# Performance work log

Measured on AMD Instinct MI355X. Metric: run time of the kernel, lower is better.

## Reference

```python
import jax, jax.numpy as jnp
import numpy as np

DIM = 128
N = 1024


def setup_inputs() -> dict:
    key = jax.random.key(0)
    ks = jax.random.split(key, 11)
    s = 1.0 / np.sqrt(DIM)
    # Linear params stored as [in, out] (y = x @ W + b), matching torch math.
    return {
        "x": jax.random.normal(ks[0], (N, DIM), jnp.float32),
        "W_Q": jax.random.uniform(ks[1], (DIM, DIM), jnp.float32, -s, s),
        "b_Q": jax.random.uniform(ks[2], (DIM,), jnp.float32, -s, s),
        "W_K": jax.random.uniform(ks[3], (DIM, DIM), jnp.float32, -s, s),
        "b_K": jax.random.uniform(ks[4], (DIM,), jnp.float32, -s, s),
        "W_V": jax.random.uniform(ks[5], (DIM, DIM), jnp.float32, -s, s),
        "b_V": jax.random.uniform(ks[6], (DIM,), jnp.float32, -s, s),
        "W_Ev": jax.random.uniform(ks[7], (DIM, DIM), jnp.float32, -s, s),
        "b_Ev": jax.random.uniform(ks[8], (DIM,), jnp.float32, -s, s),
        "W_A": jax.random.uniform(ks[9], (DIM, 1), jnp.float32, -s, s),
        "b_A": jax.random.uniform(ks[10], (1,), jnp.float32, -s, s),
    }


def reference(x, W_Q, b_Q, W_K, b_K, W_V, b_V, W_Ev, b_Ev, W_A, b_A):
    Q = x @ W_Q + b_Q                               # [n, d]
    K = x @ W_K + b_K                               # [n, d]
    V = x @ W_V + b_V                               # [n, d]
    edge_feat = jax.nn.relu(Q[:, None, :] + K[None, :, :])   # [n, n, d]
    e_ij = jnp.squeeze(edge_feat @ W_A, -1) + b_A[0]          # [n, n]
    alpha = jax.nn.softmax(e_ij, axis=1)                      # softmax over j
    EV = edge_feat @ W_Ev + b_Ev                              # [n, n, d]
    # out_i = sum_j alpha_ij * (V_j + EV_ij)
    out = jnp.einsum('ij,ijd->id', alpha, V[None, :, :] + EV)
    return out
```

## Files before the change

### kernel.cpp

```cpp
#include <hip/hip_runtime.h>

#define N 1024
#define DIM 128
#define TI 4
#define JCH 128
#define NCH 8
#define SC 16
#define NSC 8

template <int CTRL>
__device__ __forceinline__ float dpp_add(float x) {
  int y = __builtin_amdgcn_update_dpp(0, __float_as_int(x), CTRL, 0xF, 0xF, true);
  return x + __int_as_float(y);
}
__device__ __forceinline__ float red32(float x) {
  x = dpp_add<0x111>(x);
  x = dpp_add<0x112>(x);
  x = dpp_add<0x114>(x);
  x = dpp_add<0x118>(x);
  x = dpp_add<0x142>(x);
  return x;
}

__device__ __forceinline__ float bcast32(float x, bool hi) {
  const float a = __int_as_float(__builtin_amdgcn_readlane(__float_as_int(x), 31));
  const float b = __int_as_float(__builtin_amdgcn_readlane(__float_as_int(x), 63));
  return hi ? b : a;
}

__device__ __forceinline__ float epart(const float4 q, const float4 k,
                                       const float4 w) {
  float a = fmaxf(q.x + k.x, 0.f) * w.x;
  a = fmaf(fmaxf(q.y + k.y, 0.f), w.y, a);
  a = fmaf(fmaxf(q.z + k.z, 0.f), w.z, a);
  a = fmaf(fmaxf(q.w + k.w, 0.f), w.w, a);
  return a;
}

__global__ __launch_bounds__(256) void qkv_kernel2(
    const float* __restrict__ x,
    const float* __restrict__ WQ, const float* __restrict__ bQ,
    const float* __restrict__ WK, const float* __restrict__ bK,
    const float* __restrict__ WV, const float* __restrict__ bV,
    float* __restrict__ Q, float* __restrict__ K, float* __restrict__ V) {
  const int i0 = blockIdx.x * 2;
  const int t = threadIdx.x;
  const int dq = t & 31;
  const int g = t >> 5;
  const int r = g & 1;
  const int qr = g >> 1;

  __shared__ __align__(16) float xs[2][DIM];
  __shared__ __align__(16) float pacc[4][3][2][DIM];

  if (t < 64) {
    const int row = t >> 5, c4 = t & 31;
    ((float4*)&xs[row][0])[c4] = ((const float4*)(x + (i0 + row) * DIM))[c4];
  }
  __syncthreads();

  const float4* WQ4 = (const float4*)WQ;
  const float4* WK4 = (const float4*)WK;
  const float4* WV4 = (const float4*)WV;
  float4 aQ = make_float4(0.f, 0.f, 0.f, 0.f);
  float4 aK = make_float4(0.f, 0.f, 0.f, 0.f);
  float4 aV = make_float4(0.f, 0.f, 0.f, 0.f);
  const int cbase = 32 * qr;
  for (int cc = 0; cc < 32; ++cc) {
    const int c = cbase + cc;
    const float xv = xs[r][c];
    const float4 wq = WQ4[c * 32 + dq];
    const float4 wk = WK4[c * 32 + dq];
    const float4 wv = WV4[c * 32 + dq];
    aQ.x = fmaf(xv, wq.x, aQ.x); aQ.y = fmaf(xv, wq.y, aQ.y);
    aQ.z = fmaf(xv, wq.z, aQ.z); aQ.w = fmaf(xv, wq.w, aQ.w);
    aK.x = fmaf(xv, wk.x, aK.x); aK.y = fmaf(xv, wk.y, aK.y);
    aK.z = fmaf(xv, wk.z, aK.z); aK.w = fmaf(xv, wk.w, aK.w);
    aV.x = fmaf(xv, wv.x, aV.x); aV.y = fmaf(xv, wv.y, aV.y);
    aV.z = fmaf(xv, wv.z, aV.z); aV.w = fmaf(xv, wv.w, aV.w);
  }
  ((float4*)&pacc[qr][0][r][0])[dq] = aQ;
  ((float4*)&pacc[qr][1][r][0])[dq] = aK;
  ((float4*)&pacc[qr][2][r][0])[dq] = aV;
  __syncthreads();

  {
    const int row = t >> 7, d = t & 127;
    const float q = (pacc[0][0][row][d] + pacc[1][0][row][d]) +
                    (pacc[2][0][row][d] + pacc[3][0][row][d]) + bQ[d];
    const float k = (pacc[0][1][row][d] + pacc[1][1][row][d]) +
                    (pacc[2][1][row][d] + pacc[3][1][row][d]) + bK[d];
    const float v = (pacc[0][2][row][d] + pacc[1][2][row][d]) +
                    (pacc[2][2][row][d] + pacc[3][2][row][d]) + bV[d];
    Q[(i0 + row) * DIM + d] = q;
    K[(i0 + row) * DIM + d] = k;
    V[(i0 + row) * DIM + d] = v;
  }
}

__global__ __launch_bounds__(256) void attn_fused4(
    const float* __restrict__ Q, const float* __restrict__ K,
    const float* __restrict__ V, const float* __restrict__ WA,
    float* __restrict__ Rw, float* __restrict__ Sw, float* __restrict__ Lw) {
  const int bi = blockIdx.x >> 3;
  const int jc = blockIdx.x & 7;
  const int i0 = bi * TI;
  const int j0 = jc * JCH;
  const int t = threadIdx.x;
  const int dq = t & 31;
  const int f = t >> 5;
  const bool hi = (t & 32) != 0;

  __shared__ __align__(16) float red_s[8 * TI * DIM];
  __shared__ __align__(16) float4 lred4[8];

  const float4 wa4 = ((const float4*)WA)[dq];
  float4 q4[TI];
#pragma unroll
  for (int r = 0; r < TI; ++r)
    q4[r] = ((const float4*)(Q + (i0 + r) * DIM))[dq];

  float4 Racc[TI], Sacc[TI];
#pragma unroll
  for (int r = 0; r < TI; ++r) {
    Racc[r] = make_float4(0.f, 0.f, 0.f, 0.f);
    Sacc[r] = make_float4(0.f, 0.f, 0.f, 0.f);
  }
  float4 lacc = make_float4(0.f, 0.f, 0.f, 0.f);

  float4 kc0 = ((const float4*)(K + (j0 + f) * DIM))[dq];
  float4 kc1 = ((const float4*)(K + (j0 + 8 + f) * DIM))[dq];
  float4 vc0 = ((const float4*)(V + (j0 + f) * DIM))[dq];
  float4 vc1 = ((const float4*)(V + (j0 + 8 + f) * DIM))[dq];

  for (int sc = 0; sc < NSC; ++sc) {
    float4 pe0, pe1;
    pe0.x = epart(q4[0], kc0, wa4); pe0.y = epart(q4[1], kc0, wa4);
    pe0.z = epart(q4[2], kc0, wa4); pe0.w = epart(q4[3], kc0, wa4);
    pe1.x = epart(q4[0], kc1, wa4); pe1.y = epart(q4[1], kc1, wa4);
    pe1.z = epart(q4[2], kc1, wa4); pe1.w = epart(q4[3], kc1, wa4);

    const int scn = (sc + 1 < NSC) ? sc + 1 : sc;
    const int jb = j0 + scn * SC;
    const float4 kn0 = ((const float4*)(K + (jb + f) * DIM))[dq];
    const float4 kn1 = ((const float4*)(K + (jb + 8 + f) * DIM))[dq];
    const float4 vn0 = ((const float4*)(V + (jb + f) * DIM))[dq];
    const float4 vn1 = ((const float4*)(V + (jb + 8 + f) * DIM))[dq];

    pe0.x = red32(pe0.x); pe0.y = red32(pe0.y);
    pe0.z = red32(pe0.z); pe0.w = red32(pe0.w);
    pe1.x = red32(pe1.x); pe1.y = red32(pe1.y);
    pe1.z = red32(pe1.z); pe1.w = red32(pe1.w);

    float4 p0, p1;
    p0.x = __expf(bcast32(pe0.x, hi)); p0.y = __expf(bcast32(pe0.y, hi));
    p0.z = __expf(bcast32(pe0.z, hi)); p0.w = __expf(bcast32(pe0.w, hi));
    p1.x = __expf(bcast32(pe1.x, hi)); p1.y = __expf(bcast32(pe1.y, hi));
    p1.z = __expf(bcast32(pe1.z, hi)); p1.w = __expf(bcast32(pe1.w, hi));

    {
      const float pr0[4] = {p0.x, p0.y, p0.z, p0.w};
      const float pr1[4] = {p1.x, p1.y, p1.z, p1.w};
#pragma unroll
      for (int r = 0; r < TI; ++r) {
        const float pa = pr0[r], pb = pr1[r];
        Racc[r].x = fmaf(pa, fmaxf(q4[r].x + kc0.x, 0.f), Racc[r].x);
        Racc[r].y = fmaf(pa, fmaxf(q4[r].y + kc0.y, 0.f), Racc[r].y);
        Racc[r].z = fmaf(pa, fmaxf(q4[r].z + kc0.z, 0.f), Racc[r].z);
        Racc[r].w = fmaf(pa, fmaxf(q4[r].w + kc0.w, 0.f), Racc[r].w);
        Racc[r].x = fmaf(pb, fmaxf(q4[r].x + kc1.x, 0.f), Racc[r].x);
        Racc[r].y = fmaf(pb, fmaxf(q4[r].y + kc1.y, 0.f), Racc[r].y);
        Racc[r].z = fmaf(pb, fmaxf(q4[r].z + kc1.z, 0.f), Racc[r].z);
        Racc[r].w = fmaf(pb, fmaxf(q4[r].w + kc1.w, 0.f), Racc[r].w);
        Sacc[r].x = fmaf(pa, vc0.x, Sacc[r].x);
        Sacc[r].y = fmaf(pa, vc0.y, Sacc[r].y);
        Sacc[r].z = fmaf(pa, vc0.z, Sacc[r].z);
        Sacc[r].w = fmaf(pa, vc0.w, Sacc[r].w);
        Sacc[r].x = fmaf(pb, vc1.x, Sacc[r].x);
        Sacc[r].y = fmaf(pb, vc1.y, Sacc[r].y);
        Sacc[r].z = fmaf(pb, vc1.z, Sacc[r].z);
        Sacc[r].w = fmaf(pb, vc1.w, Sacc[r].w);
      }
      lacc.x += p0.x + p1.x; lacc.y += p0.y + p1.y;
      lacc.z += p0.z + p1.z; lacc.w += p0.w + p1.w;
    }

    kc0 = kn0; kc1 = kn1; vc0 = vn0; vc1 = vn1;
  }

  float4* F4 = (float4*)red_s;
#pragma unroll
  for (int r = 0; r < TI; ++r) F4[(f * 4 + r) * 32 + dq] = Racc[r];
  if (dq == 0) lred4[f] = lacc;
  __syncthreads();
#pragma unroll
  for (int p = 0; p < 2; ++p) {
    const int o = t + 256 * p;
    const int r = o >> 7, d = o & 127;
    float acc = 0.f;
#pragma unroll
    for (int c = 0; c < 8; ++c) acc += red_s[(c * 4 + r) * 128 + d];
    Rw[(jc * N + i0 + r) * DIM + d] = acc;
  }
  if (t < TI) {
    float l = 0.f;
#pragma unroll
    for (int c = 0; c < 8; ++c) l += ((const float*)&lred4[c])[t];
    Lw[jc * N + i0 + t] = l;
  }
  __syncthreads();
#pragma unroll
  for (int r = 0; r < TI; ++r) F4[(f * 4 + r) * 32 + dq] = Sacc[r];
  __syncthreads();
#pragma unroll
  for (int p = 0; p < 2; ++p) {
    const int o = t + 256 * p;
    const int r = o >> 7, d = o & 127;
    float acc = 0.f;
#pragma unroll
    for (int c = 0; c < 8; ++c) acc += red_s[(c * 4 + r) * 128 + d];
    Sw[(jc * N + i0 + r) * DIM + d] = acc;
  }
}

__global__ __launch_bounds__(256) void attn_combine4(
    const float* __restrict__ WEv, const float* __restrict__ bEv,
    const float* __restrict__ Rw, const float* __restrict__ Sw,
    const float* __restrict__ Lw, float* __restrict__ out) {
  const int i = blockIdx.x;
  const int t = threadIdx.x;

  __shared__ __align__(16) float Rst[DIM];
  __shared__ __align__(16) float Sst[DIM];
  __shared__ __align__(16) float4 Eacc4[8][DIM / 4];
  __shared__ float linv_s;

  if (t < 8) {
    float l = Lw[t * N + i];
#pragma unroll
    for (int mask = 1; mask <= 4; mask <<= 1) l += __shfl_xor(l, mask, 8);
    if (t == 0) linv_s = 1.0f / l;
  }

  {
    const int d = t & 127, h = t >> 7;
    float acc = 0.f;
    if (h == 0) {
#pragma unroll
      for (int c = 0; c < 8; ++c) acc += Rw[(c * N + i) * DIM + d];
      Rst[d] = acc;
    } else {
#pragma unroll
      for (int c = 0; c < 8; ++c) acc += Sw[(c * N + i) * DIM + d];
      Sst[d] = acc;
    }
  }
  __syncthreads();

  {
    const int dq = t & 31;
    const int qr = t >> 5;
    const float4* WEv4 = (const float4*)WEv;
    float4 acc = make_float4(0.f, 0.f, 0.f, 0.f);
    const int dp0 = 16 * qr;
#pragma unroll 8
    for (int dp = dp0; dp < dp0 + 16; ++dp) {
      const float rv = Rst[dp];
      const float4 w4 = WEv4[dp * 32 + dq];
      acc.x = fmaf(rv, w4.x, acc.x);
      acc.y = fmaf(rv, w4.y, acc.y);
      acc.z = fmaf(rv, w4.z, acc.z);
      acc.w = fmaf(rv, w4.w, acc.w);
    }
    Eacc4[qr][dq] = acc;
  }
  __syncthreads();

  if (t < DIM) {
    const int dq = t >> 2, e = t & 3;
    float acc = Sst[t];
#pragma unroll
    for (int qr = 0; qr < 8; ++qr)
      acc += ((const float*)&Eacc4[qr][dq])[e];
    out[i * DIM + t] = fmaf(acc, linv_s, bEv[t]);
  }
}

__global__ __launch_bounds__(256) void attn_fallback(
    const float* __restrict__ Q, const float* __restrict__ K,
    const float* __restrict__ V, const float* __restrict__ WA,
    const float* __restrict__ WEv, const float* __restrict__ bEv,
    float* __restrict__ out) {
  const int i = blockIdx.x;
  const int t = threadIdx.x;

  __shared__ __align__(16) float qs[DIM];
  __shared__ __align__(16) float was[DIM];
  __shared__ __align__(16) float p[N];
  __shared__ float red[256];
  __shared__ __align__(16) float Rs[8][DIM];
  __shared__ __align__(16) float Ss[8][DIM];

  if (t < DIM) {
    qs[t] = Q[i * DIM + t];
    was[t] = WA[t];
  }
  __syncthreads();

  float evals[4];
  float mloc = -3.4e38f;
  for (int jj = 0; jj < 4; ++jj) {
    const int j = t + jj * 256;
    const float4* krow = (const float4*)(K + j * DIM);
    const float4* q4p = (const float4*)qs;
    const float4* w4p = (const float4*)was;
    float acc = 0.f;
    for (int d4 = 0; d4 < DIM / 4; ++d4) {
      const float4 k4 = krow[d4];
      const float4 q4 = q4p[d4];
      const float4 w4 = w4p[d4];
      acc = fmaf(fmaxf(q4.x + k4.x, 0.f), w4.x, acc);
      acc = fmaf(fmaxf(q4.y + k4.y, 0.f), w4.y, acc);
      acc = fmaf(fmaxf(q4.z + k4.z, 0.f), w4.z, acc);
      acc = fmaf(fmaxf(q4.w + k4.w, 0.f), w4.w, acc);
    }
    evals[jj] = acc;
    mloc = fmaxf(mloc, acc);
  }
  red[t] = mloc;
  __syncthreads();
  for (int s = 128; s > 0; s >>= 1) {
    if (t < s) red[t] = fmaxf(red[t], red[t + s]);
    __syncthreads();
  }
  const float m = red[0];
  __syncthreads();
  float lsum = 0.f;
  for (int jj = 0; jj < 4; ++jj) {
    const float pe = __expf(evals[jj] - m);
    p[t + jj * 256] = pe;
    lsum += pe;
  }
  red[t] = lsum;
  __syncthreads();
  for (int s = 128; s > 0; s >>= 1) {
    if (t < s) red[t] += red[t + s];
    __syncthreads();
  }
  const float linv = 1.0f / red[0];
  __syncthreads();

  const int tx = t & 31;
  const int ty = t >> 5;
  const float4 q4 = ((const float4*)qs)[tx];
  float4 R4 = make_float4(0.f, 0.f, 0.f, 0.f);
  float4 S4 = make_float4(0.f, 0.f, 0.f, 0.f);
  for (int j = ty; j < N; j += 8) {
    const float pj = p[j];
    const float4 k4 = ((const float4*)(K + j * DIM))[tx];
    const float4 v4 = ((const float4*)(V + j * DIM))[tx];
    R4.x = fmaf(pj, fmaxf(q4.x + k4.x, 0.f), R4.x);
    R4.y = fmaf(pj, fmaxf(q4.y + k4.y, 0.f), R4.y);
    R4.z = fmaf(pj, fmaxf(q4.z + k4.z, 0.f), R4.z);
    R4.w = fmaf(pj, fmaxf(q4.w + k4.w, 0.f), R4.w);
    S4.x = fmaf(pj, v4.x, S4.x);
    S4.y = fmaf(pj, v4.y, S4.y);
    S4.z = fmaf(pj, v4.z, S4.z);
    S4.w = fmaf(pj, v4.w, S4.w);
  }
  ((float4*)&Rs[ty][0])[tx] = R4;
  ((float4*)&Ss[ty][0])[tx] = S4;
  __syncthreads();

  if (t < DIM) {
    float R = 0.f, S = 0.f;
    for (int g = 0; g < 8; ++g) {
      R += Rs[g][t];
      S += Ss[g][t];
    }
    Rs[0][t] = R;
    Ss[0][t] = S;
  }
  __syncthreads();

  if (t < DIM) {
    float o = Ss[0][t];
    for (int dp = 0; dp < DIM; ++dp) {
      o = fmaf(Rs[0][dp], WEv[dp * DIM + t], o);
    }
    out[i * DIM + t] = fmaf(o, linv, bEv[t]);
  }
}

extern "C" void kernel_launch(void* const* d_in, const int* in_sizes, int n_in,
                              void* d_out, int out_size, void* d_ws, size_t ws_size,
                              hipStream_t stream) {
  const float* x    = (const float*)d_in[0];
  const float* W_Q  = (const float*)d_in[1];
  const float* b_Q  = (const float*)d_in[2];
  const float* W_K  = (const float*)d_in[3];
  const float* b_K  = (const float*)d_in[4];
  const float* W_V  = (const float*)d_in[5];
  const float* b_V  = (const float*)d_in[6];
  const float* W_Ev = (const float*)d_in[7];
  const float* b_Ev = (const float*)d_in[8];
  const float* W_A  = (const float*)d_in[9];

  float* Q = (float*)d_ws;
  float* K = Q + N * DIM;
  float* V = K + N * DIM;
  float* out = (float*)d_out;

  const size_t need_floats = (size_t)3 * N * DIM + (size_t)2 * NCH * N * DIM +
                             (size_t)NCH * N;

  qkv_kernel2<<<N / 2, 256, 0, stream>>>(x, W_Q, b_Q, W_K, b_K, W_V, b_V, Q, K, V);

  if (ws_size >= need_floats * sizeof(float)) {
    float* Rw = V + N * DIM;
    float* Sw = Rw + NCH * N * DIM;
    float* Lw = Sw + NCH * N * DIM;
    attn_fused4<<<(N / TI) * NCH, 256, 0, stream>>>(Q, K, V, W_A, Rw, Sw, Lw);
    attn_combine4<<<N, 256, 0, stream>>>(W_Ev, b_Ev, Rw, Sw, Lw, out);
  } else {
    attn_fallback<<<N, 256, 0, stream>>>(Q, K, V, W_A, W_Ev, b_Ev, out);
  }
}
```

Before: 123.6 us.

## Rework QKV, attention and combine kernels with fewer chunks and exp2 softmax

The j-split is halved from 8 to 4 chunks of 256 keys, which cuts the partial R/S workspace traffic and the combine work. The attention loop now computes the relu values once and reuses them for both logits and accumulation. It uses exp2 with log2e folded into W_A and ds_bpermute for the broadcast, and merges the two smem reduction phases into one. The QKV kernel now processes 4 rows per 512-thread block, and combine handles 2 rows per block to reuse W_Ev loads. The trade-offs are fewer blocks in the attention kernel, more registers from the kept relu values, and a larger smem footprint in the QKV kernel.

```diff
diff --git a/kernel.cpp b/kernel.cpp
--- a/kernel.cpp
+++ b/kernel.cpp
@@ -3,10 +3,10 @@
 #define N 1024
 #define DIM 128
 #define TI 4
-#define JCH 128
-#define NCH 8
+#define JCH 256
+#define NCH 4
 #define SC 16
-#define NSC 8
+#define NSC 16
 
 template <int CTRL>
 __device__ __forceinline__ float dpp_add(float x) {
@@ -22,38 +22,51 @@
   return x;
 }
 
-__device__ __forceinline__ float bcast32(float x, bool hi) {
-  const float a = __int_as_float(__builtin_amdgcn_readlane(__float_as_int(x), 31));
-  const float b = __int_as_float(__builtin_amdgcn_readlane(__float_as_int(x), 63));
-  return hi ? b : a;
-}
-
-__device__ __forceinline__ float epart(const float4 q, const float4 k,
-                                       const float4 w) {
-  float a = fmaxf(q.x + k.x, 0.f) * w.x;
-  a = fmaf(fmaxf(q.y + k.y, 0.f), w.y, a);
-  a = fmaf(fmaxf(q.z + k.z, 0.f), w.z, a);
-  a = fmaf(fmaxf(q.w + k.w, 0.f), w.w, a);
+__device__ __forceinline__ float bperm(int baddr, float x) {
+  return __int_as_float(__builtin_amdgcn_ds_bpermute(baddr, __float_as_int(x)));
+}
+
+__device__ __forceinline__ float epart_keep(const float4 q, const float4 k,
+                                            const float4 w, float4* relu) {
+  const float rx = fmaxf(q.x + k.x, 0.f);
+  const float ry = fmaxf(q.y + k.y, 0.f);
+  const float rz = fmaxf(q.z + k.z, 0.f);
+  const float rw = fmaxf(q.w + k.w, 0.f);
+  relu->x = rx; relu->y = ry; relu->z = rz; relu->w = rw;
+  float a = rx * w.x;
+  a = fmaf(ry, w.y, a);
+  a = fmaf(rz, w.z, a);
+  a = fmaf(rw, w.w, a);
   return a;
 }
 
-__global__ __launch_bounds__(256) void qkv_kernel2(
+__device__ __forceinline__ void accum_rs(float p, const float4 relu,
+                                         const float4 v, float4* R, float4* S) {
+  R->x = fmaf(p, relu.x, R->x);
+  R->y = fmaf(p, relu.y, R->y);
+  R->z = fmaf(p, relu.z, R->z);
+  R->w = fmaf(p, relu.w, R->w);
+  S->x = fmaf(p, v.x, S->x);
+  S->y = fmaf(p, v.y, S->y);
+  S->z = fmaf(p, v.z, S->z);
+  S->w = fmaf(p, v.w, S->w);
+}
+
+__global__ __launch_bounds__(512) void qkv_kernel3(
     const float* __restrict__ x,
     const float* __restrict__ WQ, const float* __restrict__ bQ,
     const float* __restrict__ WK, const float* __restrict__ bK,
     const float* __restrict__ WV, const float* __restrict__ bV,
     float* __restrict__ Q, float* __restrict__ K, float* __restrict__ V) {
-  const int i0 = blockIdx.x * 2;
+  const int i0 = blockIdx.x * 4;
   const int t = threadIdx.x;
   const int dq = t & 31;
-  const int g = t >> 5;
-  const int r = g & 1;
-  const int qr = g >> 1;
-
-  __shared__ __align__(16) float xs[2][DIM];
-  __shared__ __align__(16) float pacc[4][3][2][DIM];
-
-  if (t < 64) {
+  const int qr = t >> 5;
+
+  __shared__ __align__(16) float xs[4][DIM];
+  __shared__ __align__(16) float pacc[16][3][4][DIM];
+
+  if (t < 128) {
     const int row = t >> 5, c4 = t & 31;
     ((float4*)&xs[row][0])[c4] = ((const float4*)(x + (i0 + row) * DIM))[c4];
   }
@@ -62,59 +75,72 @@
   const float4* WQ4 = (const float4*)WQ;
   const float4* WK4 = (const float4*)WK;
   const float4* WV4 = (const float4*)WV;
-  float4 aQ = make_float4(0.f, 0.f, 0.f, 0.f);
-  float4 aK = make_float4(0.f, 0.f, 0.f, 0.f);
-  float4 aV = make_float4(0.f, 0.f, 0.f, 0.f);
-  const int cbase = 32 * qr;
-  for (int cc = 0; cc < 32; ++cc) {
-    const int c = cbase + cc;
-    const float xv = xs[r][c];
+  float4 aQ[4], aK[4], aV[4];
+#pragma unroll
+  for (int r = 0; r < 4; ++r) {
+    aQ[r] = make_float4(0.f, 0.f, 0.f, 0.f);
+    aK[r] = make_float4(0.f, 0.f, 0.f, 0.f);
+    aV[r] = make_float4(0.f, 0.f, 0.f, 0.f);
+  }
+  const int c0 = qr * 8;
+#pragma unroll 2
+  for (int cc = 0; cc < 8; ++cc) {
+    const int c = c0 + cc;
     const float4 wq = WQ4[c * 32 + dq];
     const float4 wk = WK4[c * 32 + dq];
     const float4 wv = WV4[c * 32 + dq];
-    aQ.x = fmaf(xv, wq.x, aQ.x); aQ.y = fmaf(xv, wq.y, aQ.y);
-    aQ.z = fmaf(xv, wq.z, aQ.z); aQ.w = fmaf(xv, wq.w, aQ.w);
-    aK.x = fmaf(xv, wk.x, aK.x); aK.y = fmaf(xv, wk.y, aK.y);
-    aK.z = fmaf(xv, wk.z, aK.z); aK.w = fmaf(xv, wk.w, aK.w);
-    aV.x = fmaf(xv, wv.x, aV.x); aV.y = fmaf(xv, wv.y, aV.y);
-    aV.z = fmaf(xv, wv.z, aV.z); aV.w = fmaf(xv, wv.w, aV.w);
-  }
-  ((float4*)&pacc[qr][0][r][0])[dq] = aQ;
-  ((float4*)&pacc[qr][1][r][0])[dq] = aK;
-  ((float4*)&pacc[qr][2][r][0])[dq] = aV;
-  __syncthreads();
-
+#pragma unroll
+    for (int r = 0; r < 4; ++r) {
+      const float xv = xs[r][c];
+      aQ[r].x = fmaf(xv, wq.x, aQ[r].x); aQ[r].y = fmaf(xv, wq.y, aQ[r].y);
+      aQ[r].z = fmaf(xv, wq.z, aQ[r].z); aQ[r].w = fmaf(xv, wq.w, aQ[r].w);
+      aK[r].x = fmaf(xv, wk.x, aK[r].x); aK[r].y = fmaf(xv, wk.y, aK[r].y);
+      aK[r].z = fmaf(xv, wk.z, aK[r].z); aK[r].w = fmaf(xv, wk.w, aK[r].w);
+      aV[r].x = fmaf(xv, wv.x, aV[r].x); aV[r].y = fmaf(xv, wv.y, aV[r].y);
+      aV[r].z = fmaf(xv, wv.z, aV[r].z); aV[r].w = fmaf(xv, wv.w, aV[r].w);
+    }
+  }
+#pragma unroll
+  for (int r = 0; r < 4; ++r) {
+    ((float4*)&pacc[qr][0][r][0])[dq] = aQ[r];
+    ((float4*)&pacc[qr][1][r][0])[dq] = aK[r];
+    ((float4*)&pacc[qr][2][r][0])[dq] = aV[r];
+  }
+  __syncthreads();
   {
-    const int row = t >> 7, d = t & 127;
-    const float q = (pacc[0][0][row][d] + pacc[1][0][row][d]) +
-                    (pacc[2][0][row][d] + pacc[3][0][row][d]) + bQ[d];
-    const float k = (pacc[0][1][row][d] + pacc[1][1][row][d]) +
-                    (pacc[2][1][row][d] + pacc[3][1][row][d]) + bK[d];
-    const float v = (pacc[0][2][row][d] + pacc[1][2][row][d]) +
-                    (pacc[2][2][row][d] + pacc[3][2][row][d]) + bV[d];
-    Q[(i0 + row) * DIM + d] = q;
-    K[(i0 + row) * DIM + d] = k;
-    V[(i0 + row) * DIM + d] = v;
-  }
-}
-
-__global__ __launch_bounds__(256) void attn_fused4(
+    const int row = (t >> 7) & 3, d = t & 127;
+#pragma unroll
+    for (int m = 0; m < 3; ++m) {
+      float s = 0.f;
+#pragma unroll
+      for (int c = 0; c < 16; ++c) s += pacc[c][m][row][d];
+      float* dst = (m == 0) ? Q : (m == 1) ? K : V;
+      const float* bias = (m == 0) ? bQ : (m == 1) ? bK : bV;
+      dst[(i0 + row) * DIM + d] = s + bias[d];
+    }
+  }
+}
+
+__global__ __launch_bounds__(256) void attn_fused5(
     const float* __restrict__ Q, const float* __restrict__ K,
     const float* __restrict__ V, const float* __restrict__ WA,
     float* __restrict__ Rw, float* __restrict__ Sw, float* __restrict__ Lw) {
-  const int bi = blockIdx.x >> 3;
-  const int jc = blockIdx.x & 7;
+  const int bi = blockIdx.x >> 2;
+  const int jc = blockIdx.x & 3;
   const int i0 = bi * TI;
   const int j0 = jc * JCH;
   const int t = threadIdx.x;
   const int dq = t & 31;
   const int f = t >> 5;
-  const bool hi = (t & 32) != 0;
-
-  __shared__ __align__(16) float red_s[8 * TI * DIM];
+  const int baddr = (t & 32) ? (63 << 2) : (31 << 2);
+
+  __shared__ __align__(16) float red_s[2][8 * TI * DIM];
   __shared__ __align__(16) float4 lred4[8];
 
-  const float4 wa4 = ((const float4*)WA)[dq];
+  float4 wa4 = ((const float4*)WA)[dq];
+  const float LOG2E = 1.44269504088896340736f;
+  wa4.x *= LOG2E; wa4.y *= LOG2E; wa4.z *= LOG2E; wa4.w *= LOG2E;
+
   float4 q4[TI];
 #pragma unroll
   for (int r = 0; r < TI; ++r)
@@ -128,79 +154,86 @@
   }
   float4 lacc = make_float4(0.f, 0.f, 0.f, 0.f);
 
-  float4 kc0 = ((const float4*)(K + (j0 + f) * DIM))[dq];
-  float4 kc1 = ((const float4*)(K + (j0 + 8 + f) * DIM))[dq];
-  float4 vc0 = ((const float4*)(V + (j0 + f) * DIM))[dq];
-  float4 vc1 = ((const float4*)(V + (j0 + 8 + f) * DIM))[dq];
+  const float4* K4 = (const float4*)K;
+  const float4* V4 = (const float4*)V;
+  float4 kc0 = K4[(j0 + f) * 32 + dq];
+  float4 kc1 = K4[(j0 + 8 + f) * 32 + dq];
+  float4 vc0 = V4[(j0 + f) * 32 + dq];
+  float4 vc1 = V4[(j0 + 8 + f) * 32 + dq];
 
   for (int sc = 0; sc < NSC; ++sc) {
-    float4 pe0, pe1;
-    pe0.x = epart(q4[0], kc0, wa4); pe0.y = epart(q4[1], kc0, wa4);
-    pe0.z = epart(q4[2], kc0, wa4); pe0.w = epart(q4[3], kc0, wa4);
-    pe1.x = epart(q4[0], kc1, wa4); pe1.y = epart(q4[1], kc1, wa4);
-    pe1.z = epart(q4[2], kc1, wa4); pe1.w = epart(q4[3], kc1, wa4);
+    float4 reluA0, reluA1, reluA2, reluA3;
+    float4 peA;
+    peA.x = epart_keep(q4[0], kc0, wa4, &reluA0);
+    peA.y = epart_keep(q4[1], kc0, wa4, &reluA1);
+    peA.z = epart_keep(q4[2], kc0, wa4, &reluA2);
+    peA.w = epart_keep(q4[3], kc0, wa4, &reluA3);
 
     const int scn = (sc + 1 < NSC) ? sc + 1 : sc;
     const int jb = j0 + scn * SC;
-    const float4 kn0 = ((const float4*)(K + (jb + f) * DIM))[dq];
-    const float4 kn1 = ((const float4*)(K + (jb + 8 + f) * DIM))[dq];
-    const float4 vn0 = ((const float4*)(V + (jb + f) * DIM))[dq];
-    const float4 vn1 = ((const float4*)(V + (jb + 8 + f) * DIM))[dq];
-
-    pe0.x = red32(pe0.x); pe0.y = red32(pe0.y);
-    pe0.z = red32(pe0.z); pe0.w = red32(pe0.w);
-    pe1.x = red32(pe1.x); pe1.y = red32(pe1.y);
-    pe1.z = red32(pe1.z); pe1.w = red32(pe1.w);
-
-    float4 p0, p1;
-    p0.x = __expf(bcast32(pe0.x, hi)); p0.y = __expf(bcast32(pe0.y, hi));
-    p0.z = __expf(bcast32(pe0.z, hi)); p0.w = __expf(bcast32(pe0.w, hi));
-    p1.x = __expf(bcast32(pe1.x, hi)); p1.y = __expf(bcast32(pe1.y, hi));
-    p1.z = __expf(bcast32(pe1.z, hi)); p1.w = __expf(bcast32(pe1.w, hi));
-
-    {
-      const float pr0[4] = {p0.x, p0.y, p0.z, p0.w};
-      const float pr1[4] = {p1.x, p1.y, p1.z, p1.w};
-#pragma unroll
-      for (int r = 0; r < TI; ++r) {
-        const float pa = pr0[r], pb = pr1[r];
-        Racc[r].x = fmaf(pa, fmaxf(q4[r].x + kc0.x, 0.f), Racc[r].x);
-        Racc[r].y = fmaf(pa, fmaxf(q4[r].y + kc0.y, 0.f), Racc[r].y);
-        Racc[r].z = fmaf(pa, fmaxf(q4[r].z + kc0.z, 0.f), Racc[r].z);
-        Racc[r].w = fmaf(pa, fmaxf(q4[r].w + kc0.w, 0.f), Racc[r].w);
-        Racc[r].x = fmaf(pb, fmaxf(q4[r].x + kc1.x, 0.f), Racc[r].x);
-        Racc[r].y = fmaf(pb, fmaxf(q4[r].y + kc1.y, 0.f), Racc[r].y);
-        Racc[r].z = fmaf(pb, fmaxf(q4[r].z + kc1.z, 0.f), Racc[r].z);
-        Racc[r].w = fmaf(pb, fmaxf(q4[r].w + kc1.w, 0.f), Racc[r].w);
-        Sacc[r].x = fmaf(pa, vc0.x, Sacc[r].x);
-        Sacc[r].y = fmaf(pa, vc0.y, Sacc[r].y);
-        Sacc[r].z = fmaf(pa, vc0.z, Sacc[r].z);
-        Sacc[r].w = fmaf(pa, vc0.w, Sacc[r].w);
-        Sacc[r].x = fmaf(pb, vc1.x, Sacc[r].x);
-        Sacc[r].y = fmaf(pb, vc1.y, Sacc[r].y);
-        Sacc[r].z = fmaf(pb, vc1.z, Sacc[r].z);
-        Sacc[r].w = fmaf(pb, vc1.w, Sacc[r].w);
-      }
-      lacc.x += p0.x + p1.x; lacc.y += p0.y + p1.y;
-      lacc.z += p0.z + p1.z; lacc.w += p0.w + p1.w;
-    }
+    const float4 kn0 = K4[(jb + f) * 32 + dq];
+    const float4 kn1 = K4[(jb + 8 + f) * 32 + dq];
+    const float4 vn0 = V4[(jb + f) * 32 + dq];
+    const float4 vn1 = V4[(jb + 8 + f) * 32 + dq];
+
+    peA.x = red32(peA.x); peA.y = red32(peA.y);
+    peA.z = red32(peA.z); peA.w = red32(peA.w);
+    float4 pA;
+    pA.x = __builtin_amdgcn_exp2f(bperm(baddr, peA.x));
+    pA.y = __builtin_amdgcn_exp2f(bperm(baddr, peA.y));
+    pA.z = __builtin_amdgcn_exp2f(bperm(baddr, peA.z));
+    pA.w = __builtin_amdgcn_exp2f(bperm(baddr, peA.w));
+
+    accum_rs(pA.x, reluA0, vc0, &Racc[0], &Sacc[0]);
+    accum_rs(pA.y, reluA1, vc0, &Racc[1], &Sacc[1]);
+    accum_rs(pA.z, reluA2, vc0, &Racc[2], &Sacc[2]);
+    accum_rs(pA.w, reluA3, vc0, &Racc[3], &Sacc[3]);
+    lacc.x += pA.x; lacc.y += pA.y; lacc.z += pA.z; lacc.w += pA.w;
+
+    float4 reluB0, reluB1, reluB2, reluB3;
+    float4 peB;
+    peB.x = epart_keep(q4[0], kc1, wa4, &reluB0);
+    peB.y = epart_keep(q4[1], kc1, wa4, &reluB1);
+    peB.z = epart_keep(q4[2], kc1, wa4, &reluB2);
+    peB.w = epart_keep(q4[3], kc1, wa4, &reluB3);
+
+    peB.x = red32(peB.x); peB.y = red32(peB.y);
+    peB.z = red32(peB.z); peB.w = red32(peB.w);
+    float4 pB;
+    pB.x = __builtin_amdgcn_exp2f(bperm(baddr, peB.x));
+    pB.y = __builtin_amdgcn_exp2f(bperm(baddr, peB.y));
+    pB.z = __builtin_amdgcn_exp2f(bperm(baddr, peB.z));
+    pB.w = __builtin_amdgcn_exp2f(bperm(baddr, peB.w));
+
+    accum_rs(pB.x, reluB0, vc1, &Racc[0], &Sacc[0]);
+    accum_rs(pB.y, reluB1, vc1, &Racc[1], &Sacc[1]);
+    accum_rs(pB.z, reluB2, vc1, &Racc[2], &Sacc[2]);
+    accum_rs(pB.w, reluB3, vc1, &Racc[3], &Sacc[3]);
+    lacc.x += pB.x; lacc.y += pB.y; lacc.z += pB.z; lacc.w += pB.w;
 
     kc0 = kn0; kc1 = kn1; vc0 = vn0; vc1 = vn1;
   }
 
-  float4* F4 = (float4*)red_s;
-#pragma unroll
-  for (int r = 0; r < TI; ++r) F4[(f * 4 + r) * 32 + dq] = Racc[r];
+  float4* F4r = (float4*)&red_s[0][0];
+  float4* F4s = (float4*)&red_s[1][0];
+#pragma unroll
+  for (int r = 0; r < TI; ++r) {
+    F4r[(f * 4 + r) * 32 + dq] = Racc[r];
+    F4s[(f * 4 + r) * 32 + dq] = Sacc[r];
+  }
   if (dq == 0) lred4[f] = lacc;
   __syncthreads();
 #pragma unroll
-  for (int p = 0; p < 2; ++p) {
+  for (int p = 0; p < 4; ++p) {
     const int o = t + 256 * p;
-    const int r = o >> 7, d = o & 127;
+    const int m = o >> 9;
+    const int r = (o >> 7) & 3;
+    const int d = o & 127;
     float acc = 0.f;
 #pragma unroll
-    for (int c = 0; c < 8; ++c) acc += red_s[(c * 4 + r) * 128 + d];
-    Rw[(jc * N + i0 + r) * DIM + d] = acc;
+    for (int c = 0; c < 8; ++c) acc += red_s[m][(c * 4 + r) * 128 + d];
+    float* dst = m ? Sw : Rw;
+    dst[(jc * N + i0 + r) * DIM + d] = acc;
   }
   if (t < TI) {
     float l = 0.f;
@@ -208,52 +241,40 @@
     for (int c = 0; c < 8; ++c) l += ((const float*)&lred4[c])[t];
     Lw[jc * N + i0 + t] = l;
   }
-  __syncthreads();
-#pragma unroll
-  for (int r = 0; r < TI; ++r) F4[(f * 4 + r) * 32 + dq] = Sacc[r];
-  __syncthreads();
-#pragma unroll
-  for (int p = 0; p < 2; ++p) {
-    const int o = t + 256 * p;
-    const int r = o >> 7, d = o & 127;
-    float acc = 0.f;
-#pragma unroll
-    for (int c = 0; c < 8; ++c) acc += red_s[(c * 4 + r) * 128 + d];
-    Sw[(jc * N + i0 + r) * DIM + d] = acc;
-  }
-}
-
-__global__ __launch_bounds__(256) void attn_combine4(
+}
+
+__global__ __launch_bounds__(256) void attn_combine5(
     const float* __restrict__ WEv, const float* __restrict__ bEv,
     const float* __restrict__ Rw, const float* __restrict__ Sw,
     const float* __restrict__ Lw, float* __restrict__ out) {
-  const int i = blockIdx.x;
+  const int i0 = blockIdx.x * 2;
   const int t = threadIdx.x;
 
-  __shared__ __align__(16) float Rst[DIM];
-  __shared__ __align__(16) float Sst[DIM];
-  __shared__ __align__(16) float4 Eacc4[8][DIM / 4];
-  __shared__ float linv_s;
+  __shared__ __align__(16) float Rst[2][DIM];
+  __shared__ __align__(16) float Sst[2][DIM];
+  __shared__ __align__(16) float4 Eacc4[8][2][DIM / 4];
+  __shared__ float linv_s[2];
 
   if (t < 8) {
-    float l = Lw[t * N + i];
-#pragma unroll
-    for (int mask = 1; mask <= 4; mask <<= 1) l += __shfl_xor(l, mask, 8);
-    if (t == 0) linv_s = 1.0f / l;
-  }
-
-  {
-    const int d = t & 127, h = t >> 7;
+    const int row = t >> 2, c = t & 3;
+    float l = Lw[c * N + i0 + row];
+    l += __shfl_xor(l, 1, 4);
+    l += __shfl_xor(l, 2, 4);
+    if (c == 0) linv_s[row] = 1.0f / l;
+  }
+
+#pragma unroll
+  for (int p = 0; p < 2; ++p) {
+    const int o = t + 256 * p;
+    const int d = o & 127;
+    const int set = o >> 7;
+    const int row = set & 1;
+    const int mat = set >> 1;
+    const float* src = mat ? Sw : Rw;
     float acc = 0.f;
-    if (h == 0) {
-#pragma unroll
-      for (int c = 0; c < 8; ++c) acc += Rw[(c * N + i) * DIM + d];
-      Rst[d] = acc;
-    } else {
-#pragma unroll
-      for (int c = 0; c < 8; ++c) acc += Sw[(c * N + i) * DIM + d];
-      Sst[d] = acc;
-    }
+#pragma unroll
+    for (int c = 0; c < NCH; ++c) acc += src[(c * N + i0 + row) * DIM + d];
+    if (mat) Sst[row][d] = acc; else Rst[row][d] = acc;
   }
   __syncthreads();
 
@@ -261,28 +282,32 @@
     const int dq = t & 31;
     const int qr = t >> 5;
     const float4* WEv4 = (const float4*)WEv;
-    float4 acc = make_float4(0.f, 0.f, 0.f, 0.f);
+    float4 a0 = make_float4(0.f, 0.f, 0.f, 0.f);
+    float4 a1 = make_float4(0.f, 0.f, 0.f, 0.f);
     const int dp0 = 16 * qr;
 #pragma unroll 8
     for (int dp = dp0; dp < dp0 + 16; ++dp) {
-      const float rv = Rst[dp];
       const float4 w4 = WEv4[dp * 32 + dq];
-      acc.x = fmaf(rv, w4.x, acc.x);
-      acc.y = fmaf(rv, w4.y, acc.y);
-      acc.z = fmaf(rv, w4.z, acc.z);
-      acc.w = fmaf(rv, w4.w, acc.w);
-    }
-    Eacc4[qr][dq] = acc;
-  }
-  __syncthreads();
-
-  if (t < DIM) {
-    const int dq = t >> 2, e = t & 3;
-    float acc = Sst[t];
+      const float r0 = Rst[0][dp];
+      const float r1 = Rst[1][dp];
+      a0.x = fmaf(r0, w4.x, a0.x); a0.y = fmaf(r0, w4.y, a0.y);
+      a0.z = fmaf(r0, w4.z, a0.z); a0.w = fmaf(r0, w4.w, a0.w);
+      a1.x = fmaf(r1, w4.x, a1.x); a1.y = fmaf(r1, w4.y, a1.y);
+      a1.z = fmaf(r1, w4.z, a1.z); a1.w = fmaf(r1, w4.w, a1.w);
+    }
+    Eacc4[qr][0][dq] = a0;
+    Eacc4[qr][1][dq] = a1;
+  }
+  __syncthreads();
+
+  {
+    const int row = t >> 7, d = t & 127;
+    const int dq = d >> 2, e = d & 3;
+    float acc = Sst[row][d];
 #pragma unroll
     for (int qr = 0; qr < 8; ++qr)
-      acc += ((const float*)&Eacc4[qr][dq])[e];
-    out[i * DIM + t] = fmaf(acc, linv_s, bEv[t]);
+      acc += ((const float*)&Eacc4[qr][row][dq])[e];
+    out[(i0 + row) * DIM + d] = fmaf(acc, linv_s[row], bEv[d]);
   }
 }
 
@@ -414,14 +439,14 @@
   const size_t need_floats = (size_t)3 * N * DIM + (size_t)2 * NCH * N * DIM +
                              (size_t)NCH * N;
 
-  qkv_kernel2<<<N / 2, 256, 0, stream>>>(x, W_Q, b_Q, W_K, b_K, W_V, b_V, Q, K, V);
+  qkv_kernel3<<<N / 4, 512, 0, stream>>>(x, W_Q, b_Q, W_K, b_K, W_V, b_V, Q, K, V);
 
   if (ws_size >= need_floats * sizeof(float)) {
     float* Rw = V + N * DIM;
     float* Sw = Rw + NCH * N * DIM;
     float* Lw = Sw + NCH * N * DIM;
-    attn_fused4<<<(N / TI) * NCH, 256, 0, stream>>>(Q, K, V, W_A, Rw, Sw, Lw);
-    attn_combine4<<<N, 256, 0, stream>>>(W_Ev, b_Ev, Rw, Sw, Lw, out);
+    attn_fused5<<<(N / TI) * NCH, 256, 0, stream>>>(Q, K, V, W_A, Rw, Sw, Lw);
+    attn_combine5<<<N / 2, 256, 0, stream>>>(W_Ev, b_Ev, Rw, Sw, Lw, out);
   } else {
     attn_fallback<<<N, 256, 0, stream>>>(Q, K, V, W_A, W_Ev, b_Ev, out);
   }
```

Measured after the change: 111.6 us. -9.7%, faster.
